# Kernel optimization log

Hardware: AMD Instinct MI355X
Metric: run time of the kernel (lower is better)

The kernel has to match this reference:

```python
import jax, jax.numpy as jnp
import numpy as np

V = 49688; D = 128; Hd = 256; DM = 2 * Hd; FF = 4 * Hd; NH = 4
B = 256; O = 32; L = 32

def _ln(x, g, b, eps=1e-5):
    m = x.mean(-1, keepdims=True)
    v = x.var(-1, keepdims=True)
    return (x - m) / jnp.sqrt(v + eps) * g + b

def _mha(x, in_w, in_b, out_w, out_b, nh):
    Bx, S, E = x.shape
    hd = E // nh
    qkv = x @ in_w.T + in_b
    q, k, v = jnp.split(qkv, 3, axis=-1)
    sp = lambda t: t.reshape(Bx, S, nh, hd).transpose(0, 2, 1, 3)
    q, k, v = sp(q), sp(k), sp(v)
    s = jnp.einsum('bhqd,bhkd->bhqk', q, k) / jnp.sqrt(jnp.asarray(hd, x.dtype))
    o = jnp.einsum('bhqk,bhkd->bhqd', jax.nn.softmax(s, -1), v)
    o = o.transpose(0, 2, 1, 3).reshape(Bx, S, E)
    return o @ out_w.T + out_b

def _gru_dir(x, wih, whh, bih, bhh):
    Bx, T, _ = x.shape
    H = whh.shape[1]
    def step(h, xt):
        gi = xt @ wih.T + bih
        gh = h @ whh.T + bhh
        ir, iz, inn = jnp.split(gi, 3, -1)
        hr, hz, hn = jnp.split(gh, 3, -1)
        r = jax.nn.sigmoid(ir + hr)
        z = jax.nn.sigmoid(iz + hz)
        n = jnp.tanh(inn + r * hn)
        h = (1 - z) * n + z * h
        return h, h
    _, hs = jax.lax.scan(step, jnp.zeros((Bx, H), x.dtype), jnp.swapaxes(x, 0, 1))
    return jnp.swapaxes(hs, 0, 1)

def setup_inputs():
    key = jax.random.key(0)
    it = iter(jax.random.split(key, 48))
    def nrm(shape, s=0.05):
        return jax.random.normal(next(it), shape, jnp.float32) * s
    inp = {}
    inp['order_history'] = jax.random.randint(next(it), (B, O, L), 0, V + 1)
    inp['days_between'] = jax.random.uniform(next(it), (B, O - 1), jnp.float32) * 30.0
    inp['days_since_last'] = jax.random.uniform(next(it), (B,), jnp.float32) * 30.0
    inp['emb'] = nrm((V + 1, D), 1.0).at[0].set(0.0)  # padding_idx=0 -> zero row
    inp['a_in_w'] = nrm((3 * D, D)); inp['a_in_b'] = jnp.zeros((3 * D,))
    inp['a_out_w'] = nrm((D, D)); inp['a_out_b'] = jnp.zeros((D,))
    for d in ('f', 'b'):
        inp['g_wih_' + d] = nrm((3 * Hd, D)); inp['g_whh_' + d] = nrm((3 * Hd, Hd))
        inp['g_bih_' + d] = jnp.zeros((3 * Hd,)); inp['g_bhh_' + d] = jnp.zeros((3 * Hd,))
    inp['t_in_w'] = nrm((3 * DM, DM)); inp['t_in_b'] = jnp.zeros((3 * DM,))
    inp['t_out_w'] = nrm((DM, DM)); inp['t_out_b'] = jnp.zeros((DM,))
    inp['t_ln1_g'] = jnp.ones((DM,)); inp['t_ln1_b'] = jnp.zeros((DM,))
    inp['t_ff1_w'] = nrm((FF, DM)); inp['t_ff1_b'] = jnp.zeros((FF,))
    inp['t_ff2_w'] = nrm((DM, FF)); inp['t_ff2_b'] = jnp.zeros((DM,))
    inp['t_ln2_g'] = jnp.ones((DM,)); inp['t_ln2_b'] = jnp.zeros((DM,))
    inp['te1_w'] = nrm((Hd // 4, 2)); inp['te1_b'] = jnp.zeros((Hd // 4,))
    inp['te_ln1_g'] = jnp.ones((Hd // 4,)); inp['te_ln1_b'] = jnp.zeros((Hd // 4,))
    inp['te2_w'] = nrm((Hd // 2, Hd // 4)); inp['te2_b'] = jnp.zeros((Hd // 2,))
    inp['te_ln2_g'] = jnp.ones((Hd // 2,)); inp['te_ln2_b'] = jnp.zeros((Hd // 2,))
    inp['c_w'] = nrm((Hd, 2 * Hd + Hd // 2)); inp['c_b'] = jnp.zeros((Hd,))
    inp['c_ln_g'] = jnp.ones((Hd,)); inp['c_ln_b'] = jnp.zeros((Hd,))
    return inp

def reference(order_history, days_between, days_since_last, emb, a_in_w, a_in_b, a_out_w, a_out_b, g_wih_f, g_whh_f, g_bih_f, g_bhh_f, g_wih_b, g_whh_b, g_bih_b, g_bhh_b, t_in_w, t_in_b, t_out_w, t_out_b, t_ln1_g, t_ln1_b, t_ff1_w, t_ff1_b, t_ff2_w, t_ff2_b, t_ln2_g, t_ln2_b, te1_w, te1_b, te_ln1_g, te_ln1_b, te2_w, te2_b, te_ln2_g, te_ln2_b, c_w, c_b, c_ln_g, c_ln_b):
    Bx, Ox, Lx = order_history.shape
    # per-order item self-attention, batched over all (user, order) pairs
    x = emb[order_history].reshape(Bx * Ox, Lx, -1)                  # [B*O, L, D]
    x = _mha(x, a_in_w, a_in_b, a_out_w, a_out_b, NH)
    order_emb = x.mean(1).reshape(Bx, Ox, -1)                        # [B, O, D]
    # bidirectional GRU over the order sequence
    hf = _gru_dir(order_emb, g_wih_f, g_whh_f, g_bih_f, g_bhh_f)
    hb = _gru_dir(order_emb[:, ::-1], g_wih_b, g_whh_b, g_bih_b, g_bhh_b)[:, ::-1]
    g = jnp.concatenate([hf, hb], -1)                                # [B, O, 2H]
    # post-LN TransformerEncoderLayer (relu, dropout in eval mode)
    a = _mha(g, t_in_w, t_in_b, t_out_w, t_out_b, NH)
    g = _ln(g + a, t_ln1_g, t_ln1_b)
    f = jax.nn.relu(g @ t_ff1_w.T + t_ff1_b) @ t_ff2_w.T + t_ff2_b
    g = _ln(g + f, t_ln2_g, t_ln2_b)
    enc = g.mean(1)                                                  # [B, 2H]
    # temporal features: only days_mean and recency are used (std computed but unused in original)
    feats = jnp.stack([days_between.mean(1), days_since_last], 1)    # [B, 2]
    te = jax.nn.relu(_ln(feats @ te1_w.T + te1_b, te_ln1_g, te_ln1_b))
    te = jax.nn.relu(_ln(te @ te2_w.T + te2_b, te_ln2_g, te_ln2_b))  # [B, H/2]
    out = jax.nn.relu(_ln(jnp.concatenate([enc, te], 1) @ c_w.T + c_b, c_ln_g, c_ln_b))
    return out                                                       # [B, H]
```

## Files before the change

kernel.cpp:

```cpp
#include <hip/hip_runtime.h>
#include <hip/hip_bf16.h>
#include <math.h>

typedef __hip_bfloat16 bf16;
typedef __attribute__((ext_vector_type(8))) short short8v;
typedef __attribute__((ext_vector_type(4))) short short4v;
typedef __attribute__((ext_vector_type(4))) float float4v;
#define MFMA16 __builtin_amdgcn_mfma_f32_16x16x32_bf16

__device__ __forceinline__ float us2f(unsigned short u) {
  union { unsigned u; float f; } c; c.u = ((unsigned)u) << 16; return c.f;
}
__device__ __forceinline__ unsigned short f2us(float f) {
  return __bfloat16_as_ushort(__float2bfloat16(f));
}

__device__ __forceinline__ float dot_ff(const float* __restrict__ x,
                                        const float* __restrict__ w, int K) {
  const float4* xp = reinterpret_cast<const float4*>(x);
  const float4* wp = reinterpret_cast<const float4*>(w);
  float acc = 0.f;
  const int n = K >> 2;
  for (int i = 0; i < n; ++i) {
    float4 a = xp[i], b = wp[i];
    acc += a.x*b.x + a.y*b.y + a.z*b.z + a.w*b.w;
  }
  return acc;
}

__device__ __forceinline__ float sigm(float x) { return 1.f / (1.f + __expf(-x)); }
__device__ __forceinline__ float tanh_fast(float x) {
  x = fminf(fmaxf(x, -15.f), 15.f);
  float e = __expf(2.f * x);
  return (e - 1.f) / (e + 1.f);
}

__global__ void k_canary(float* __restrict__ out) {
  out[blockIdx.x * 256 + threadIdx.x] = 100.0f;
}

__global__ __launch_bounds__(256) void k_cvt(
    const float* __restrict__ a_in_w, const float* __restrict__ t_in_w,
    const float* __restrict__ t_out_w, const float* __restrict__ t_ff1w,
    const float* __restrict__ t_ff2w, const float* __restrict__ a_out_w,
    unsigned short* __restrict__ awb, unsigned short* __restrict__ twb,
    unsigned short* __restrict__ pwb, unsigned short* __restrict__ f1wb,
    unsigned short* __restrict__ f2wb, unsigned short* __restrict__ awb2)
{
  int i = blockIdx.x * 256 + threadIdx.x;
  if (i < 49152)  awb[i] = f2us(a_in_w[i]);
  if (i < 786432) twb[i] = f2us(t_in_w[i]);
  if (i < 262144) pwb[i] = f2us(t_out_w[i]);
  if (i < 524288) f1wb[i] = f2us(t_ff1w[i]);
  if (i < 524288) f2wb[i] = f2us(t_ff2w[i]);
  if (i < 16384)  awb2[i] = f2us(a_out_w[i]);
}

__global__ __launch_bounds__(256) void k_gru_wb(
    const float* __restrict__ wih_f, const float* __restrict__ whh_f,
    const float* __restrict__ wih_b, const float* __restrict__ whh_b,
    unsigned short* __restrict__ whhb, unsigned short* __restrict__ wihb)
{
  int i = blockIdx.x * 256 + threadIdx.x;
  if (i >= 393216) return;
  int dir = i / 196608, r = i % 196608;
  whhb[i] = f2us((dir ? whh_b : whh_f)[r]);
  if (r < 98304) wihb[dir * 98304 + r] = f2us((dir ? wih_b : wih_f)[r]);
}

__global__ __launch_bounds__(256, 2) void k_qkvpre(
    const float* __restrict__ emb, const unsigned short* __restrict__ awb,
    const float* __restrict__ in_b,
    unsigned short* __restrict__ qkt, unsigned short* __restrict__ vt)
{
  const int row0 = blockIdx.x * 32, tid = threadIdx.x;
  __shared__ alignas(16) unsigned short xs[32 * 136];
  for (int i = tid; i < 1024; i += 256) {
    int t = i >> 5, c4 = (i & 31) << 2;
    int grow = row0 + t; if (grow > 49688) grow = 49688;
    float4 e4 = *reinterpret_cast<const float4*>(emb + (size_t)grow * 128 + c4);
    short4v s; s[0] = f2us(e4.x); s[1] = f2us(e4.y); s[2] = f2us(e4.z); s[3] = f2us(e4.w);
    *reinterpret_cast<short4v*>(xs + t * 136 + c4) = s;
  }
  __syncthreads();
  const int lane = tid & 63, wave = tid >> 6;
  const int l15 = lane & 15, quad = lane >> 4;
  short8v af[2][4];
#pragma unroll
  for (int mt = 0; mt < 2; ++mt)
#pragma unroll
    for (int kc = 0; kc < 4; ++kc)
      af[mt][kc] = *reinterpret_cast<const short8v*>(
          xs + (mt * 16 + l15) * 136 + kc * 32 + quad * 8);
  for (int ni = 0; ni < 6; ++ni) {
    const int j = (wave + ni * 4) * 16 + l15;
    const unsigned short* wrow = awb + (size_t)j * 128;
    float4v acc0 = {0.f, 0.f, 0.f, 0.f}, acc1 = {0.f, 0.f, 0.f, 0.f};
#pragma unroll
    for (int kc = 0; kc < 4; ++kc) {
      short8v bfr = *reinterpret_cast<const short8v*>(wrow + kc * 32 + quad * 8);
      acc0 = MFMA16(af[0][kc], bfr, acc0, 0, 0, 0);
      acc1 = MFMA16(af[1][kc], bfr, acc1, 0, 0, 0);
    }
    const float bj = in_b[j];
#pragma unroll
    for (int r = 0; r < 4; ++r) {
      int g0 = row0 + quad * 4 + r, g1 = g0 + 16;
      if (j < 256) {
        if (g0 <= 49688) qkt[(size_t)g0 * 256 + j] = f2us(acc0[r] + bj);
        if (g1 <= 49688) qkt[(size_t)g1 * 256 + j] = f2us(acc1[r] + bj);
      } else {
        int jj = j - 256;
        if (g0 <= 49688) vt[(size_t)g0 * 128 + jj] = f2us(acc0[r] + bj);
        if (g1 <= 49688) vt[(size_t)g1 * 128 + jj] = f2us(acc1[r] + bj);
      }
    }
  }
}

__global__ __launch_bounds__(256, 5) void k_order_attn(
    const int* __restrict__ oh, const unsigned short* __restrict__ qkt,
    const unsigned short* __restrict__ vt,
    const unsigned short* __restrict__ awb2, const float* __restrict__ out_b,
    unsigned short* __restrict__ oeb)
{
  const int bo = blockIdx.x;
  const int tid = threadIdx.x;
  __shared__ alignas(16) unsigned short qb[32 * 136];
  __shared__ alignas(16) unsigned short kb[32 * 136];
  __shared__ alignas(16) unsigned short vTb[128 * 32];
  unsigned short* ob = qb;
  unsigned short* pb = kb;

  const int lane = tid & 63, wave = tid >> 6;
  const int l15 = lane & 15, quad = lane >> 4;

  for (int i = tid; i < 1024; i += 256) {
    int t = i >> 5, c8 = (i & 31) << 3;
    int id = oh[bo * 32 + t];
    short8v v8 = *reinterpret_cast<const short8v*>(qkt + (size_t)id * 256 + c8);
    if (c8 < 128) *reinterpret_cast<short8v*>(qb + t * 136 + c8) = v8;
    else          *reinterpret_cast<short8v*>(kb + t * 136 + (c8 - 128)) = v8;
  }
  for (int i = tid; i < 512; i += 256) {
    int t = i & 31, c8 = (i >> 5) << 3;
    int id = oh[bo * 32 + t];
    short8v v8 = *reinterpret_cast<const short8v*>(vt + (size_t)id * 128 + c8);
#pragma unroll
    for (int j2 = 0; j2 < 8; ++j2) vTb[(c8 + j2) * 32 + t] = v8[j2];
  }
  __syncthreads();
  {
    const int h = wave;
    const float scale1 = 0.17677669529663687f;
    short8v qf[2], kf[2];
#pragma unroll
    for (int mt = 0; mt < 2; ++mt)
      qf[mt] = *reinterpret_cast<const short8v*>(qb + (mt * 16 + l15) * 136 + h * 32 + quad * 8);
#pragma unroll
    for (int nt = 0; nt < 2; ++nt)
      kf[nt] = *reinterpret_cast<const short8v*>(kb + (nt * 16 + l15) * 136 + h * 32 + quad * 8);
    float4v sacc[2][2];
#pragma unroll
    for (int mt = 0; mt < 2; ++mt)
#pragma unroll
      for (int nt = 0; nt < 2; ++nt) {
        sacc[mt][nt] = (float4v){0.f, 0.f, 0.f, 0.f};
        sacc[mt][nt] = MFMA16(qf[mt], kf[nt], sacc[mt][nt], 0, 0, 0);
      }
    __syncthreads();
#pragma unroll
    for (int mt = 0; mt < 2; ++mt)
#pragma unroll
      for (int r = 0; r < 4; ++r) {
        float e0 = __expf(sacc[mt][0][r] * scale1);
        float e1 = __expf(sacc[mt][1][r] * scale1);
        int row = h * 32 + mt * 16 + quad * 4 + r;
        pb[row * 32 + l15] = f2us(e0);
        pb[row * 32 + 16 + l15] = f2us(e1);
      }
    short8v ones;
#pragma unroll
    for (int i = 0; i < 8; ++i) ones[i] = (short)0x3F80;
    short8v pf[2], vf[2];
#pragma unroll
    for (int mt = 0; mt < 2; ++mt)
      pf[mt] = *reinterpret_cast<const short8v*>(pb + (h * 32 + mt * 16 + l15) * 32 + quad * 8);
    float4v sums[2];
#pragma unroll
    for (int mt = 0; mt < 2; ++mt) {
      sums[mt] = (float4v){0.f, 0.f, 0.f, 0.f};
      sums[mt] = MFMA16(pf[mt], ones, sums[mt], 0, 0, 0);
    }
#pragma unroll
    for (int nt = 0; nt < 2; ++nt)
      vf[nt] = *reinterpret_cast<const short8v*>(vTb + (h * 32 + nt * 16 + l15) * 32 + quad * 8);
    float4v oacc[2][2];
#pragma unroll
    for (int mt = 0; mt < 2; ++mt)
#pragma unroll
      for (int nt = 0; nt < 2; ++nt) {
        oacc[mt][nt] = (float4v){0.f, 0.f, 0.f, 0.f};
        oacc[mt][nt] = MFMA16(pf[mt], vf[nt], oacc[mt][nt], 0, 0, 0);
      }
#pragma unroll
    for (int mt = 0; mt < 2; ++mt)
#pragma unroll
      for (int r = 0; r < 4; ++r) {
        int t = mt * 16 + quad * 4 + r;
        float inv = 1.f / sums[mt][r];
#pragma unroll
        for (int nt = 0; nt < 2; ++nt)
          ob[t * 136 + h * 32 + nt * 16 + l15] = f2us(oacc[mt][nt][r] * inv);
      }
  }
  __syncthreads();
  {
    float4v acc[2][2];
#pragma unroll
    for (int mt = 0; mt < 2; ++mt)
#pragma unroll
      for (int nt = 0; nt < 2; ++nt) acc[mt][nt] = (float4v){0.f, 0.f, 0.f, 0.f};
#pragma unroll
    for (int kc = 0; kc < 4; ++kc) {
      short8v af0 = *reinterpret_cast<const short8v*>(ob + l15 * 136 + kc * 32 + quad * 8);
      short8v af1 = *reinterpret_cast<const short8v*>(ob + (16 + l15) * 136 + kc * 32 + quad * 8);
#pragma unroll
      for (int nt = 0; nt < 2; ++nt) {
        int j = (wave * 2 + nt) * 16 + l15;
        short8v bfr = *reinterpret_cast<const short8v*>(awb2 + (size_t)j * 128 + kc * 32 + quad * 8);
        acc[0][nt] = MFMA16(af0, bfr, acc[0][nt], 0, 0, 0);
        acc[1][nt] = MFMA16(af1, bfr, acc[1][nt], 0, 0, 0);
      }
    }
#pragma unroll
    for (int nt = 0; nt < 2; ++nt) {
      float part = 0.f;
#pragma unroll
      for (int mt = 0; mt < 2; ++mt)
#pragma unroll
        for (int r = 0; r < 4; ++r) part += acc[mt][nt][r];
      part += __shfl_xor(part, 16);
      part += __shfl_xor(part, 32);
      if (quad == 0) {
        int j = (wave * 2 + nt) * 16 + l15;
        oeb[(size_t)bo * 128 + j] = f2us(part * (1.f / 32.f) + out_b[j]);
      }
    }
  }
}

__global__ __launch_bounds__(256, 2) void k_gru_gi(
    const unsigned short* __restrict__ oeb, const unsigned short* __restrict__ wihb,
    unsigned short* __restrict__ gi)
{
  const int row0 = blockIdx.x * 32, tid = threadIdx.x;
  __shared__ alignas(16) unsigned short xs[32 * 136];
  for (int i = tid; i < 512; i += 256) {
    int t = i >> 4, c8 = (i & 15) << 3;
    *reinterpret_cast<short8v*>(xs + t * 136 + c8) =
        *reinterpret_cast<const short8v*>(oeb + (size_t)(row0 + t) * 128 + c8);
  }
  __syncthreads();
  const int lane = tid & 63, wave = tid >> 6;
  const int l15 = lane & 15, quad = lane >> 4;
  short8v af[2][4];
#pragma unroll
  for (int mt = 0; mt < 2; ++mt)
#pragma unroll
    for (int kc = 0; kc < 4; ++kc)
      af[mt][kc] = *reinterpret_cast<const short8v*>(
          xs + (mt * 16 + l15) * 136 + kc * 32 + quad * 8);
  for (int ni = 0; ni < 24; ++ni) {
    int col = (wave + ni * 4) * 16 + l15;
    const unsigned short* wrow = wihb + (size_t)col * 128;
    float4v a0 = {0.f,0.f,0.f,0.f}, a1 = {0.f,0.f,0.f,0.f};
#pragma unroll
    for (int kc = 0; kc < 4; ++kc) {
      short8v bfr = *reinterpret_cast<const short8v*>(wrow + kc * 32 + quad * 8);
      a0 = MFMA16(af[0][kc], bfr, a0, 0, 0, 0);
      a1 = MFMA16(af[1][kc], bfr, a1, 0, 0, 0);
    }
#pragma unroll
    for (int r = 0; r < 4; ++r) {
      gi[(size_t)(row0 + quad * 4 + r) * 1536 + col] = f2us(a0[r]);
      gi[(size_t)(row0 + quad * 4 + r + 16) * 1536 + col] = f2us(a1[r]);
    }
  }
}

__global__ __launch_bounds__(512, 2) void k_gru_rec(
    const unsigned short* __restrict__ gi, const unsigned short* __restrict__ whhb,
    const float* __restrict__ bih_f, const float* __restrict__ bhh_f,
    const float* __restrict__ bih_b, const float* __restrict__ bhh_b,
    float* __restrict__ g)
{
  const int b0 = blockIdx.x * 2, dir = blockIdx.y;
  const int tid = threadIdx.x;
  const unsigned short* wb = whhb + (size_t)dir * 196608;
  const float* bih = dir ? bih_b : bih_f;
  const float* bhh = dir ? bhh_b : bhh_f;
  __shared__ alignas(16) unsigned short hb[16 * 264];
  __shared__ float pg[2 * 772];
  const int lane = tid & 63, wave = tid >> 6;
  const int l15 = lane & 15, quad = lane >> 4;
  const int j = tid & 255, mb = tid >> 8;
  const float bir = bih[j], biz = bih[256 + j], bin_ = bih[512 + j];
  const float bhr = bhh[j], bhz = bhh[256 + j], bhn  = bhh[512 + j];
  short8v wf[6][8];
  int cols[6];
#pragma unroll
  for (int ni = 0; ni < 6; ++ni) {
    cols[ni] = (wave + ni * 8) * 16 + l15;
#pragma unroll
    for (int kc = 0; kc < 8; ++kc)
      wf[ni][kc] = *reinterpret_cast<const short8v*>(
          wb + (size_t)cols[ni] * 256 + kc * 32 + quad * 8);
  }
  for (int i = tid; i < 16 * 264; i += 512) hb[i] = 0;
  int tcur = dir ? 31 : 0;
  size_t gbase = ((size_t)(b0 + mb) * 32 + tcur) * 1536 + dir * 768;
  float gr = us2f(gi[gbase + j]);
  float gz = us2f(gi[gbase + 256 + j]);
  float gn = us2f(gi[gbase + 512 + j]);
  __syncthreads();
  for (int s = 0; s < 32; ++s) {
    float4v acc[6];
#pragma unroll
    for (int ni = 0; ni < 6; ++ni) acc[ni] = (float4v){0.f, 0.f, 0.f, 0.f};
#pragma unroll
    for (int kc = 0; kc < 8; ++kc) {
      short8v af = *reinterpret_cast<const short8v*>(hb + l15 * 264 + kc * 32 + quad * 8);
#pragma unroll
      for (int ni = 0; ni < 6; ++ni)
        acc[ni] = MFMA16(af, wf[ni][kc], acc[ni], 0, 0, 0);
    }
    if (quad == 0) {
#pragma unroll
      for (int ni = 0; ni < 6; ++ni) {
        pg[cols[ni]] = acc[ni][0];
        pg[772 + cols[ni]] = acc[ni][1];
      }
    }
    float gr2 = 0.f, gz2 = 0.f, gn2 = 0.f;
    if (s < 31) {
      int t2 = dir ? (30 - s) : (s + 1);
      size_t gb2 = ((size_t)(b0 + mb) * 32 + t2) * 1536 + dir * 768;
      gr2 = us2f(gi[gb2 + j]);
      gz2 = us2f(gi[gb2 + 256 + j]);
      gn2 = us2f(gi[gb2 + 512 + j]);
    }
    __syncthreads();
    {
      const int tt = dir ? (31 - s) : s;
      float hprev = us2f(hb[mb * 264 + j]);
      float r = sigm(gr + bir + pg[mb * 772 + j] + bhr);
      float z = sigm(gz + biz + pg[mb * 772 + 256 + j] + bhz);
      float n = tanh_fast(gn + bin_ + r * (pg[mb * 772 + 512 + j] + bhn));
      float nh = (1.f - z) * n + z * hprev;
      hb[mb * 264 + j] = f2us(nh);
      g[((size_t)(b0 + mb) * 32 + tt) * 512 + dir * 256 + j] = nh;
    }
    gr = gr2; gz = gz2; gn = gn2;
    __syncthreads();
  }
}

__global__ __launch_bounds__(256, 4) void k_mha2f(
    const float* __restrict__ g, const unsigned short* __restrict__ twb,
    const float* __restrict__ Bv, float* __restrict__ attn)
{
  const int b = blockIdx.x, h = blockIdx.y, tid = threadIdx.x;
  __shared__ alignas(16) unsigned short xs3[32 * 136];
  __shared__ alignas(16) unsigned short qk[2 * 32 * 136];
  __shared__ alignas(16) unsigned short vT[128 * 40];
  unsigned short* qs = qk;
  unsigned short* ks = qk + 32 * 136;
  unsigned short* pb = xs3;
  const int lane = tid & 63, wave = tid >> 6;
  const int l15 = lane & 15, quad = lane >> 4;

  int wrowi[6];
#pragma unroll
  for (int ni = 0; ni < 6; ++ni) {
    int idx = (wave + ni * 4) * 16 + l15;
    int m = idx >> 7, dd = idx & 127;
    wrowi[ni] = m * 512 + h * 128 + dd;
  }
  float4v acc[6][2];
#pragma unroll
  for (int ni = 0; ni < 6; ++ni)
#pragma unroll
    for (int mt = 0; mt < 2; ++mt) acc[ni][mt] = (float4v){0.f, 0.f, 0.f, 0.f};

  for (int ck = 0; ck < 4; ++ck) {
    __syncthreads();
    for (int i = tid; i < 1024; i += 256) {
      int t = i >> 5, c4 = (i & 31) << 2;
      float4 e4 = *reinterpret_cast<const float4*>(
          g + (size_t)b * 16384 + t * 512 + ck * 128 + c4);
      short4v s; s[0] = f2us(e4.x); s[1] = f2us(e4.y); s[2] = f2us(e4.z); s[3] = f2us(e4.w);
      *reinterpret_cast<short4v*>(xs3 + t * 136 + c4) = s;
    }
    __syncthreads();
    short8v af2[2][4];
#pragma unroll
    for (int mt = 0; mt < 2; ++mt)
#pragma unroll
      for (int u = 0; u < 4; ++u)
        af2[mt][u] = *reinterpret_cast<const short8v*>(
            xs3 + (mt * 16 + l15) * 136 + u * 32 + quad * 8);
#pragma unroll
    for (int ni = 0; ni < 6; ++ni) {
      const unsigned short* wrow = twb + (size_t)wrowi[ni] * 512 + ck * 128;
#pragma unroll
      for (int u = 0; u < 4; ++u) {
        short8v bfr = *reinterpret_cast<const short8v*>(wrow + u * 32 + quad * 8);
        acc[ni][0] = MFMA16(af2[0][u], bfr, acc[ni][0], 0, 0, 0);
        acc[ni][1] = MFMA16(af2[1][u], bfr, acc[ni][1], 0, 0, 0);
      }
    }
  }
  __syncthreads();
#pragma unroll
  for (int ni = 0; ni < 6; ++ni) {
    int idx = (wave + ni * 4) * 16 + l15;
    int m = idx >> 7, dd = idx & 127;
    float bj = Bv[wrowi[ni]];
    if (m < 2) {
      unsigned short* dst = (m == 0) ? qs : ks;
#pragma unroll
      for (int r = 0; r < 4; ++r) {
        int t0 = quad * 4 + r;
        dst[t0 * 136 + dd] = f2us(acc[ni][0][r] + bj);
        dst[(t0 + 16) * 136 + dd] = f2us(acc[ni][1][r] + bj);
      }
    } else {
      short4v s0, s1;
#pragma unroll
      for (int r = 0; r < 4; ++r) { s0[r] = f2us(acc[ni][0][r] + bj); s1[r] = f2us(acc[ni][1][r] + bj); }
      *reinterpret_cast<short4v*>(vT + dd * 40 + quad * 4) = s0;
      *reinterpret_cast<short4v*>(vT + dd * 40 + 16 + quad * 4) = s1;
    }
  }
  __syncthreads();
  {
    const float scale2 = 0.08838834764831845f;
    const int mt = wave >> 1, nt = wave & 1;
    float4v a = {0.f, 0.f, 0.f, 0.f};
#pragma unroll
    for (int kc = 0; kc < 4; ++kc) {
      short8v qf = *reinterpret_cast<const short8v*>(qs + (mt * 16 + l15) * 136 + kc * 32 + quad * 8);
      short8v kf = *reinterpret_cast<const short8v*>(ks + (nt * 16 + l15) * 136 + kc * 32 + quad * 8);
      a = MFMA16(qf, kf, a, 0, 0, 0);
    }
#pragma unroll
    for (int r = 0; r < 4; ++r) {
      int row = mt * 16 + quad * 4 + r;
      pb[row * 32 + nt * 16 + l15] = f2us(__expf(a[r] * scale2));
    }
  }
  __syncthreads();
  {
    short8v ones;
#pragma unroll
    for (int i = 0; i < 8; ++i) ones[i] = (short)0x3F80;
    short8v pf[2], vf[2];
#pragma unroll
    for (int mt = 0; mt < 2; ++mt)
      pf[mt] = *reinterpret_cast<const short8v*>(pb + (mt * 16 + l15) * 32 + quad * 8);
    float4v sums[2];
#pragma unroll
    for (int mt = 0; mt < 2; ++mt) {
      sums[mt] = (float4v){0.f, 0.f, 0.f, 0.f};
      sums[mt] = MFMA16(pf[mt], ones, sums[mt], 0, 0, 0);
    }
#pragma unroll
    for (int ntl = 0; ntl < 2; ++ntl)
      vf[ntl] = *reinterpret_cast<const short8v*>(vT + ((2 * wave + ntl) * 16 + l15) * 40 + quad * 8);
    float4v oacc[2][2];
#pragma unroll
    for (int mt = 0; mt < 2; ++mt)
#pragma unroll
      for (int ntl = 0; ntl < 2; ++ntl) {
        oacc[mt][ntl] = (float4v){0.f, 0.f, 0.f, 0.f};
        oacc[mt][ntl] = MFMA16(pf[mt], vf[ntl], oacc[mt][ntl], 0, 0, 0);
      }
#pragma unroll
    for (int mt = 0; mt < 2; ++mt)
#pragma unroll
      for (int r = 0; r < 4; ++r) {
        int q = mt * 16 + quad * 4 + r;
        float inv = 1.f / sums[mt][r];
#pragma unroll
        for (int ntl = 0; ntl < 2; ++ntl)
          attn[((size_t)b * 32 + q) * 512 + h * 128 + (2 * wave + ntl) * 16 + l15] =
              oacc[mt][ntl][r] * inv;
      }
  }
}

__global__ __launch_bounds__(1024, 1) void k_proj(
    const float* __restrict__ X, const unsigned short* __restrict__ Wb,
    const float* __restrict__ bias, float* __restrict__ praw)
{
  const int row0 = blockIdx.x * 32, tid = threadIdx.x;
  __shared__ alignas(16) unsigned short xs[32 * 520];
  const int lane = tid & 63, wave = tid >> 6;
  const int l15 = lane & 15, quad = lane >> 4;
  for (int i = tid; i < 4096; i += 1024) {
    int t = i >> 7, c4 = (i & 127) << 2;
    float4 e4 = *reinterpret_cast<const float4*>(X + (size_t)(row0 + t) * 512 + c4);
    short4v s; s[0] = f2us(e4.x); s[1] = f2us(e4.y); s[2] = f2us(e4.z); s[3] = f2us(e4.w);
    *reinterpret_cast<short4v*>(xs + t * 520 + c4) = s;
  }
  __syncthreads();
#pragma unroll
  for (int ni = 0; ni < 2; ++ni) {
    const int col = (wave + ni * 16) * 16 + l15;
    const unsigned short* wrow = Wb + (size_t)col * 512;
    float4v a0 = {0.f,0.f,0.f,0.f}, a1 = {0.f,0.f,0.f,0.f};
#pragma unroll
    for (int kc = 0; kc < 16; ++kc) {
      short8v b = *reinterpret_cast<const short8v*>(wrow + kc * 32 + quad * 8);
      short8v x0 = *reinterpret_cast<const short8v*>(xs + l15 * 520 + kc * 32 + quad * 8);
      short8v x1 = *reinterpret_cast<const short8v*>(xs + (16 + l15) * 520 + kc * 32 + quad * 8);
      a0 = MFMA16(x0, b, a0, 0, 0, 0);
      a1 = MFMA16(x1, b, a1, 0, 0, 0);
    }
    const float bj = bias[col];
#pragma unroll
    for (int r = 0; r < 4; ++r) {
      praw[(size_t)(row0 + quad * 4 + r) * 512 + col] = a0[r] + bj;
      praw[(size_t)(row0 + 16 + quad * 4 + r) * 512 + col] = a1[r] + bj;
    }
  }
}

__global__ __launch_bounds__(1024, 1) void k_ff(
    const float* __restrict__ X, const unsigned short* __restrict__ W1,
    const float* __restrict__ b1, const unsigned short* __restrict__ W2,
    const float* __restrict__ b2, float* __restrict__ yraw)
{
  const int row0 = blockIdx.x * 32, tid = threadIdx.x;
  __shared__ alignas(16) unsigned short xs[32 * 520];
  __shared__ alignas(16) unsigned short f1c[32 * 264];
  const int lane = tid & 63, wave = tid >> 6;
  const int l15 = lane & 15, quad = lane >> 4;
  for (int i = tid; i < 4096; i += 1024) {
    int t = i >> 7, c4 = (i & 127) << 2;
    float4 e4 = *reinterpret_cast<const float4*>(X + (size_t)(row0 + t) * 512 + c4);
    short4v s; s[0] = f2us(e4.x); s[1] = f2us(e4.y); s[2] = f2us(e4.z); s[3] = f2us(e4.w);
    *reinterpret_cast<short4v*>(xs + t * 520 + c4) = s;
  }
  __syncthreads();
  float4v acc2[2][2];
#pragma unroll
  for (int mt = 0; mt < 2; ++mt)
#pragma unroll
    for (int ni = 0; ni < 2; ++ni) acc2[mt][ni] = (float4v){0.f,0.f,0.f,0.f};
  int cols2[2];
#pragma unroll
  for (int ni = 0; ni < 2; ++ni) cols2[ni] = (wave + ni * 16) * 16 + l15;

  for (int ck = 0; ck < 4; ++ck) {
    {
      const int col = ck * 256 + wave * 16 + l15;
      const unsigned short* wrow = W1 + (size_t)col * 512;
      float4v a0 = {0.f,0.f,0.f,0.f}, a1 = {0.f,0.f,0.f,0.f};
#pragma unroll
      for (int kc = 0; kc < 16; ++kc) {
        short8v b = *reinterpret_cast<const short8v*>(wrow + kc * 32 + quad * 8);
        short8v x0 = *reinterpret_cast<const short8v*>(xs + l15 * 520 + kc * 32 + quad * 8);
        short8v x1 = *reinterpret_cast<const short8v*>(xs + (16 + l15) * 520 + kc * 32 + quad * 8);
        a0 = MFMA16(x0, b, a0, 0, 0, 0);
        a1 = MFMA16(x1, b, a1, 0, 0, 0);
      }
      const float bj = b1[col];
      const int cl = wave * 16 + l15;
#pragma unroll
      for (int r = 0; r < 4; ++r) {
        f1c[(quad * 4 + r) * 264 + cl] = f2us(fmaxf(a0[r] + bj, 0.f));
        f1c[(16 + quad * 4 + r) * 264 + cl] = f2us(fmaxf(a1[r] + bj, 0.f));
      }
    }
    __syncthreads();
#pragma unroll
    for (int ni = 0; ni < 2; ++ni) {
      const unsigned short* wrow2 = W2 + (size_t)cols2[ni] * 1024 + ck * 256;
#pragma unroll
      for (int kc = 0; kc < 8; ++kc) {
        short8v b = *reinterpret_cast<const short8v*>(wrow2 + kc * 32 + quad * 8);
        short8v a0 = *reinterpret_cast<const short8v*>(f1c + l15 * 264 + kc * 32 + quad * 8);
        short8v a1 = *reinterpret_cast<const short8v*>(f1c + (16 + l15) * 264 + kc * 32 + quad * 8);
        acc2[0][ni] = MFMA16(a0, b, acc2[0][ni], 0, 0, 0);
        acc2[1][ni] = MFMA16(a1, b, acc2[1][ni], 0, 0, 0);
      }
    }
    __syncthreads();
  }
#pragma unroll
  for (int mt = 0; mt < 2; ++mt)
#pragma unroll
    for (int ni = 0; ni < 2; ++ni) {
      int col = cols2[ni];
      float bj = b2[col];
#pragma unroll
      for (int r = 0; r < 4; ++r)
        yraw[(size_t)(row0 + mt * 16 + quad * 4 + r) * 512 + col] = acc2[mt][ni][r] + bj;
    }
}

__global__ __launch_bounds__(256, 2) void k_resln(
    const float* __restrict__ yraw, const float* __restrict__ res,
    const float* __restrict__ gam, const float* __restrict__ bet,
    float* __restrict__ Y)
{
  const int row0 = blockIdx.x * 16, tid = threadIdx.x;
  __shared__ float ys[16 * 516];
  for (int i = tid; i < 16 * 512; i += 256) {
    int t = i >> 9, c = i & 511;
    ys[t * 516 + c] = yraw[(size_t)(row0 + t) * 512 + c] +
                      res[(size_t)(row0 + t) * 512 + c];
  }
  __syncthreads();
  {
    int row = tid >> 4, l16 = tid & 15;
    const float* yr = ys + row * 516;
    float part = 0.f;
#pragma unroll
    for (int k = 0; k < 32; ++k) part += yr[l16 + 16 * k];
#pragma unroll
    for (int off = 8; off; off >>= 1) part += __shfl_xor(part, off, 16);
    float mean = part * (1.f / 512.f);
    float var = 0.f;
#pragma unroll
    for (int k = 0; k < 32; ++k) { float d = yr[l16 + 16 * k] - mean; var += d * d; }
#pragma unroll
    for (int off = 8; off; off >>= 1) var += __shfl_xor(var, off, 16);
    float rs = rsqrtf(var * (1.f / 512.f) + 1e-5f);
    for (int k = 0; k < 32; ++k) {
      int c = l16 + 16 * k;
      Y[(size_t)(row0 + row) * 512 + c] = (yr[c] - mean) * rs * gam[c] + bet[c];
    }
  }
}

__global__ __launch_bounds__(256) void k_final(
    const float* __restrict__ g2,
    const float* __restrict__ db, const float* __restrict__ dsl,
    const float* __restrict__ te1_w, const float* __restrict__ te1_b,
    const float* __restrict__ l1g, const float* __restrict__ l1b,
    const float* __restrict__ te2_w, const float* __restrict__ te2_b,
    const float* __restrict__ l2g, const float* __restrict__ l2b,
    const float* __restrict__ c_w, const float* __restrict__ c_b,
    const float* __restrict__ clg, const float* __restrict__ clb,
    float* __restrict__ out)
{
  const int b = blockIdx.x, tid = threadIdx.x;
  __shared__ float cat[640];
  __shared__ float t1[64];
  __shared__ float t2[128];
  __shared__ float pre[256];
  __shared__ float red[256];
  __shared__ float st[2];
  for (int i = tid; i < 512; i += 256) {
    float acc = 0.f;
#pragma unroll
    for (int t = 0; t < 32; ++t) acc += g2[((size_t)b * 32 + t) * 512 + i];
    cat[i] = acc * (1.f / 32.f);
  }
  if (tid == 0) {
    float s = 0.f;
    for (int i = 0; i < 31; ++i) s += db[b * 31 + i];
    st[0] = s / 31.f;
    st[1] = dsl[b];
  }
  __syncthreads();
  const float f0 = st[0], f1v = st[1];
  if (tid < 64)
    t1[tid] = f0 * te1_w[tid * 2] + f1v * te1_w[tid * 2 + 1] + te1_b[tid];
  __syncthreads();
  if (tid == 0) {
    float m = 0.f; for (int i = 0; i < 64; ++i) m += t1[i]; m *= (1.f / 64.f);
    float v = 0.f; for (int i = 0; i < 64; ++i) { float d = t1[i] - m; v += d * d; }
    st[0] = m; st[1] = rsqrtf(v * (1.f / 64.f) + 1e-5f);
  }
  __syncthreads();
  if (tid < 64) {
    float v = (t1[tid] - st[0]) * st[1] * l1g[tid] + l1b[tid];
    t1[tid] = fmaxf(v, 0.f);
  }
  __syncthreads();
  if (tid < 128)
    t2[tid] = dot_ff(t1, te2_w + (size_t)tid * 64, 64) + te2_b[tid];
  __syncthreads();
  if (tid == 0) {
    float m = 0.f; for (int i = 0; i < 128; ++i) m += t2[i]; m *= (1.f / 128.f);
    float v = 0.f; for (int i = 0; i < 128; ++i) { float d = t2[i] - m; v += d * d; }
    st[0] = m; st[1] = rsqrtf(v * (1.f / 128.f) + 1e-5f);
  }
  __syncthreads();
  if (tid < 128) {
    float v = (t2[tid] - st[0]) * st[1] * l2g[tid] + l2b[tid];
    cat[512 + tid] = fmaxf(v, 0.f);
  }
  __syncthreads();
  pre[tid] = dot_ff(cat, c_w + (size_t)tid * 640, 640) + c_b[tid];
  red[tid] = pre[tid];
  __syncthreads();
  for (int s = 128; s > 0; s >>= 1) { if (tid < s) red[tid] += red[tid + s]; __syncthreads(); }
  const float m = red[0] * (1.f / 256.f);
  __syncthreads();
  const float d = pre[tid] - m;
  red[tid] = d * d;
  __syncthreads();
  for (int s = 128; s > 0; s >>= 1) { if (tid < s) red[tid] += red[tid + s]; __syncthreads(); }
  const float rs = rsqrtf(red[0] * (1.f / 256.f) + 1e-5f);
  float v = d * rs * clg[tid] + clb[tid];
  out[(size_t)b * 256 + tid] = fmaxf(v, 0.f);
}

extern "C" void kernel_launch(void* const* d_in, const int* in_sizes, int n_in,
                              void* d_out, int out_size, void* d_ws, size_t ws_size,
                              hipStream_t stream) {
  (void)in_sizes; (void)n_in; (void)out_size; (void)ws_size;
  const int*   oh     = (const int*)  d_in[0];
  const float* db     = (const float*)d_in[1];
  const float* dsl    = (const float*)d_in[2];
  const float* emb    = (const float*)d_in[3];
  const float* a_in_w = (const float*)d_in[4];
  const float* a_in_b = (const float*)d_in[5];
  const float* a_out_w= (const float*)d_in[6];
  const float* a_out_b= (const float*)d_in[7];
  const float* wih_f  = (const float*)d_in[8];
  const float* whh_f  = (const float*)d_in[9];
  const float* bih_f  = (const float*)d_in[10];
  const float* bhh_f  = (const float*)d_in[11];
  const float* wih_b  = (const float*)d_in[12];
  const float* whh_b  = (const float*)d_in[13];
  const float* bih_b  = (const float*)d_in[14];
  const float* bhh_b  = (const float*)d_in[15];
  const float* t_in_w = (const float*)d_in[16];
  const float* t_in_b = (const float*)d_in[17];
  const float* t_out_w= (const float*)d_in[18];
  const float* t_out_b= (const float*)d_in[19];
  const float* t_ln1g = (const float*)d_in[20];
  const float* t_ln1b = (const float*)d_in[21];
  const float* t_ff1w = (const float*)d_in[22];
  const float* t_ff1b = (const float*)d_in[23];
  const float* t_ff2w = (const float*)d_in[24];
  const float* t_ff2b = (const float*)d_in[25];
  const float* t_ln2g = (const float*)d_in[26];
  const float* t_ln2b = (const float*)d_in[27];
  const float* te1_w  = (const float*)d_in[28];
  const float* te1_b  = (const float*)d_in[29];
  const float* tl1g   = (const float*)d_in[30];
  const float* tl1b   = (const float*)d_in[31];
  const float* te2_w  = (const float*)d_in[32];
  const float* te2_b  = (const float*)d_in[33];
  const float* tl2g   = (const float*)d_in[34];
  const float* tl2b   = (const float*)d_in[35];
  const float* c_w    = (const float*)d_in[36];
  const float* c_b    = (const float*)d_in[37];
  const float* clng   = (const float*)d_in[38];
  const float* clnb   = (const float*)d_in[39];

  float* ws = (float*)d_ws;
  unsigned short* oeb  = (unsigned short*)ws;
  unsigned short* qkt  = (unsigned short*)(ws + 1048576);
  float* g    = ws + 1048576;
  float* yraw = ws + 1048576;
  float* attn = ws + 5242880;
  float* g1   = attn;
  float* g2   = attn;
  unsigned short* whhb = (unsigned short*)(ws + 9437184);
  unsigned short* wihb = (unsigned short*)(ws + 9633792);
  unsigned short* awb2 = (unsigned short*)(ws + 9732096);
  unsigned short* awb  = (unsigned short*)(ws + 10027008);
  unsigned short* twb  = (unsigned short*)(ws + 10051584);
  unsigned short* pwb  = (unsigned short*)(ws + 10444800);
  unsigned short* f1wb = (unsigned short*)(ws + 10575872);
  unsigned short* f2wb = (unsigned short*)(ws + 10838016);
  unsigned short* vt   = (unsigned short*)(ws + 11100160);
  unsigned short* gi   = (unsigned short*)(ws + 11100160);
  float* praw = ws + 11100160;

  k_canary<<<256, 256, 0, stream>>>((float*)d_out);
  k_cvt<<<3072, 256, 0, stream>>>(a_in_w, t_in_w, t_out_w, t_ff1w, t_ff2w, a_out_w,
                                  awb, twb, pwb, f1wb, f2wb, awb2);
  k_gru_wb<<<1536, 256, 0, stream>>>(wih_f, whh_f, wih_b, whh_b, whhb, wihb);
  k_qkvpre<<<1553, 256, 0, stream>>>(emb, awb, a_in_b, qkt, vt);
  k_order_attn<<<8192, 256, 0, stream>>>(oh, qkt, vt, awb2, a_out_b, oeb);
  k_gru_gi<<<256, 256, 0, stream>>>(oeb, wihb, gi);
  k_gru_rec<<<dim3(128, 2), 512, 0, stream>>>(gi, whhb, bih_f, bhh_f, bih_b, bhh_b, g);
  k_mha2f<<<dim3(256, 4), 256, 0, stream>>>(g, twb, t_in_b, attn);
  k_proj<<<256, 1024, 0, stream>>>(attn, pwb, t_out_b, praw);
  k_resln<<<512, 256, 0, stream>>>(praw, g, t_ln1g, t_ln1b, g1);
  k_ff<<<256, 1024, 0, stream>>>(g1, f1wb, t_ff1b, f2wb, t_ff2b, yraw);
  k_resln<<<512, 256, 0, stream>>>(yraw, g1, t_ln2g, t_ln2b, g2);
  k_final<<<256, 256, 0, stream>>>(g2, db, dsl, te1_w, te1_b, tl1g, tl1b,
                                   te2_w, te2_b, tl2g, tl2b, c_w, c_b, clng, clnb,
                                   (float*)d_out);
}
```

Measured before the change: 520.7 us.

## Split FF hidden dimension across two blocks and sum partials in layernorm

The FFN kernel now launches two blocks per 32-row tile, each covering half of the 1024-wide hidden dimension, and writes partial outputs to two buffers. A new residual-layernorm kernel adds both partials to the residual before normalizing. This doubles the block count to improve CU occupancy and latency hiding. The cost is an extra partial-sum write and read, plus loading the input tile twice.

```diff
diff --git a/kernel.cpp b/kernel.cpp
--- a/kernel.cpp
+++ b/kernel.cpp
@@ -537,12 +537,15 @@
   }
 }
 
-__global__ __launch_bounds__(1024, 1) void k_ff(
+__global__ __launch_bounds__(1024, 2) void k_ff(
     const float* __restrict__ X, const unsigned short* __restrict__ W1,
     const float* __restrict__ b1, const unsigned short* __restrict__ W2,
-    const float* __restrict__ b2, float* __restrict__ yraw)
-{
-  const int row0 = blockIdx.x * 32, tid = threadIdx.x;
+    const float* __restrict__ b2,
+    float* __restrict__ yp0, float* __restrict__ yp1)
+{
+  const int row0 = (blockIdx.x >> 1) * 32;
+  const int kh = blockIdx.x & 1;
+  const int tid = threadIdx.x;
   __shared__ alignas(16) unsigned short xs[32 * 520];
   __shared__ alignas(16) unsigned short f1c[32 * 264];
   const int lane = tid & 63, wave = tid >> 6;
@@ -563,9 +566,9 @@
 #pragma unroll
   for (int ni = 0; ni < 2; ++ni) cols2[ni] = (wave + ni * 16) * 16 + l15;
 
-  for (int ck = 0; ck < 4; ++ck) {
+  for (int ck = 0; ck < 2; ++ck) {
     {
-      const int col = ck * 256 + wave * 16 + l15;
+      const int col = kh * 512 + ck * 256 + wave * 16 + l15;
       const unsigned short* wrow = W1 + (size_t)col * 512;
       float4v a0 = {0.f,0.f,0.f,0.f}, a1 = {0.f,0.f,0.f,0.f};
 #pragma unroll
@@ -587,7 +590,7 @@
     __syncthreads();
 #pragma unroll
     for (int ni = 0; ni < 2; ++ni) {
-      const unsigned short* wrow2 = W2 + (size_t)cols2[ni] * 1024 + ck * 256;
+      const unsigned short* wrow2 = W2 + (size_t)cols2[ni] * 1024 + kh * 512 + ck * 256;
 #pragma unroll
       for (int kc = 0; kc < 8; ++kc) {
         short8v b = *reinterpret_cast<const short8v*>(wrow2 + kc * 32 + quad * 8);
@@ -599,15 +602,16 @@
     }
     __syncthreads();
   }
+  float* yp = kh ? yp1 : yp0;
 #pragma unroll
   for (int mt = 0; mt < 2; ++mt)
 #pragma unroll
     for (int ni = 0; ni < 2; ++ni) {
       int col = cols2[ni];
-      float bj = b2[col];
+      float bj = kh ? 0.f : b2[col];
 #pragma unroll
       for (int r = 0; r < 4; ++r)
-        yraw[(size_t)(row0 + mt * 16 + quad * 4 + r) * 512 + col] = acc2[mt][ni][r] + bj;
+        yp[(size_t)(row0 + mt * 16 + quad * 4 + r) * 512 + col] = acc2[mt][ni][r] + bj;
     }
 }
 
@@ -622,6 +626,42 @@
     int t = i >> 9, c = i & 511;
     ys[t * 516 + c] = yraw[(size_t)(row0 + t) * 512 + c] +
                       res[(size_t)(row0 + t) * 512 + c];
+  }
+  __syncthreads();
+  {
+    int row = tid >> 4, l16 = tid & 15;
+    const float* yr = ys + row * 516;
+    float part = 0.f;
+#pragma unroll
+    for (int k = 0; k < 32; ++k) part += yr[l16 + 16 * k];
+#pragma unroll
+    for (int off = 8; off; off >>= 1) part += __shfl_xor(part, off, 16);
+    float mean = part * (1.f / 512.f);
+    float var = 0.f;
+#pragma unroll
+    for (int k = 0; k < 32; ++k) { float d = yr[l16 + 16 * k] - mean; var += d * d; }
+#pragma unroll
+    for (int off = 8; off; off >>= 1) var += __shfl_xor(var, off, 16);
+    float rs = rsqrtf(var * (1.f / 512.f) + 1e-5f);
+    for (int k = 0; k < 32; ++k) {
+      int c = l16 + 16 * k;
+      Y[(size_t)(row0 + row) * 512 + c] = (yr[c] - mean) * rs * gam[c] + bet[c];
+    }
+  }
+}
+
+__global__ __launch_bounds__(256, 2) void k_resln2(
+    const float* __restrict__ y0, const float* __restrict__ y1,
+    const float* __restrict__ res,
+    const float* __restrict__ gam, const float* __restrict__ bet,
+    float* __restrict__ Y)
+{
+  const int row0 = blockIdx.x * 16, tid = threadIdx.x;
+  __shared__ float ys[16 * 516];
+  for (int i = tid; i < 16 * 512; i += 256) {
+    int t = i >> 9, c = i & 511;
+    size_t idx = (size_t)(row0 + t) * 512 + c;
+    ys[t * 516 + c] = y0[idx] + y1[idx] + res[idx];
   }
   __syncthreads();
   {
@@ -770,7 +810,7 @@
   unsigned short* oeb  = (unsigned short*)ws;
   unsigned short* qkt  = (unsigned short*)(ws + 1048576);
   float* g    = ws + 1048576;
-  float* yraw = ws + 1048576;
+  float* yp0  = ws + 1048576;
   float* attn = ws + 5242880;
   float* g1   = attn;
   float* g2   = attn;
@@ -785,6 +825,7 @@
   unsigned short* vt   = (unsigned short*)(ws + 11100160);
   unsigned short* gi   = (unsigned short*)(ws + 11100160);
   float* praw = ws + 11100160;
+  float* yp1  = ws + 11100160;
 
   k_canary<<<256, 256, 0, stream>>>((float*)d_out);
   k_cvt<<<3072, 256, 0, stream>>>(a_in_w, t_in_w, t_out_w, t_ff1w, t_ff2w, a_out_w,
@@ -797,8 +838,8 @@
   k_mha2f<<<dim3(256, 4), 256, 0, stream>>>(g, twb, t_in_b, attn);
   k_proj<<<256, 1024, 0, stream>>>(attn, pwb, t_out_b, praw);
   k_resln<<<512, 256, 0, stream>>>(praw, g, t_ln1g, t_ln1b, g1);
-  k_ff<<<256, 1024, 0, stream>>>(g1, f1wb, t_ff1b, f2wb, t_ff2b, yraw);
-  k_resln<<<512, 256, 0, stream>>>(yraw, g1, t_ln2g, t_ln2b, g2);
+  k_ff<<<512, 1024, 0, stream>>>(g1, f1wb, t_ff1b, f2wb, t_ff2b, yp0, yp1);
+  k_resln2<<<512, 256, 0, stream>>>(yp0, yp1, g1, t_ln2g, t_ln2b, g2);
   k_final<<<256, 256, 0, stream>>>(g2, db, dsl, te1_w, te1_b, tl1g, tl1b,
                                    te2_w, te2_b, tl2g, tl2b, c_w, c_b, clng, clnb,
                                    (float*)d_out);
```

New measurement: 528.0 us. Within noise of the previous version (+1.4%).
